# Optimization experiments

Hardware: AMD Instinct MI355X
Metric: run time of the kernel (lower is better)

Reference implementation:

```python
import jax, jax.numpy as jnp
import numpy as np

EPS_DIST = 1e-10
BN_EPS = 1e-5
K = 3  # nsample / three_nn


def setup_inputs() -> dict:
    key = jax.random.key(0)
    ks = jax.random.split(key, 8)
    B, N, S, D1, D2 = 4, 8192, 2048, 128, 256
    C_in = D1 + D2  # 384
    H = 256
    inp = {
        "pos1": jax.random.normal(ks[0], (B, 3, N), dtype=jnp.float32),
        "pos2": jax.random.normal(ks[1], (B, 3, S), dtype=jnp.float32),
        "feature1": jax.random.normal(ks[2], (B, D1, N), dtype=jnp.float32),
        "feature2": jax.random.normal(ks[3], (B, D2, S), dtype=jnp.float32),
        # MLP layer 1: Conv1d(384->256, k=1) + BN
        "W1": jax.random.normal(ks[4], (H, C_in), dtype=jnp.float32) * (1.0 / np.sqrt(C_in)),
        "b1": jnp.zeros((H,), dtype=jnp.float32),
        "g1": jnp.ones((H,), dtype=jnp.float32),
        "be1": jnp.zeros((H,), dtype=jnp.float32),
        # MLP layer 2: Conv1d(256->256, k=1) + BN
        "W2": jax.random.normal(ks[5], (H, H), dtype=jnp.float32) * (1.0 / np.sqrt(H)),
        "b2": jnp.zeros((H,), dtype=jnp.float32),
        "g2": jnp.ones((H,), dtype=jnp.float32),
        "be2": jnp.zeros((H,), dtype=jnp.float32),
    }
    return inp


def _conv_bn_relu(x, W, b, gamma, beta):
    # x: [B, Cin, N]; 1x1 Conv1d == channel GEMM
    y = jnp.einsum("oc,bcn->bon", W, x) + b[None, :, None]
    # BatchNorm1d in training mode: batch statistics over (B, N)
    mean = jnp.mean(y, axis=(0, 2), keepdims=True)
    var = jnp.mean(jnp.square(y - mean), axis=(0, 2), keepdims=True)
    y = (y - mean) * jax.lax.rsqrt(var + BN_EPS)
    y = y * gamma[None, :, None] + beta[None, :, None]
    return jax.nn.relu(y)


def reference(pos1, pos2, feature1, feature2, W1, b1, g1, be1, W2, b2, g2, be2):
    # pos1: [B,3,N], pos2: [B,3,S], feature1: [B,D1,N], feature2: [B,D2,S]
    p1 = jnp.swapaxes(pos1, 1, 2)  # [B,N,3]
    p2 = jnp.swapaxes(pos2, 1, 2)  # [B,S,3]
    # three_nn: squared-distance 3-NN of each point in p1 among p2
    d2 = (jnp.sum(p1 * p1, -1)[:, :, None]
          + jnp.sum(p2 * p2, -1)[:, None, :]
          - 2.0 * jnp.einsum("bnc,bsc->bns", p1, p2))  # [B,N,S]
    neg_vals, idx = jax.lax.top_k(-d2, K)  # idx: [B,N,3]
    dists = jnp.maximum(-neg_vals, EPS_DIST)  # dists[dists<1e-10]=1e-10
    w = 1.0 / dists
    w = w / jnp.sum(w, -1, keepdims=True)  # [B,N,3]
    # grouping_operation: gather feature2 [B,D,S] by idx -> [B,D,N,3]
    grouped = jax.vmap(lambda f, i: f[:, i])(feature2, idx)
    interpolated = jnp.sum(grouped * w[:, None, :, :], axis=-1)  # [B,D2,N]
    feat = jnp.concatenate([interpolated, feature1], axis=1)  # [B,384,N]
    feat = _conv_bn_relu(feat, W1, b1, g1, be1)
    feat = _conv_bn_relu(feat, W2, b2, g2, be2)
    return feat  # [B,256,N]
```

## Files before the change

### kernel.cpp

```cpp
#include <hip/hip_runtime.h>
#include <hip/hip_bf16.h>
#include <cstdint>

typedef unsigned short u16;
typedef unsigned int u32;
typedef unsigned long long u64;
typedef __bf16 bf16x8 __attribute__((ext_vector_type(8)));
typedef float f32x4 __attribute__((ext_vector_type(4)));
typedef u16 u16x8 __attribute__((ext_vector_type(8)));

#define FPSCALE 1048576.0f
#define FPINV   (1.0f / 1048576.0f)
#define NSLICE 16

__device__ __forceinline__ u16 f2b(float f) {
    unsigned int u = __float_as_uint(f);
    u += 0x7fffu + ((u >> 16) & 1u);
    return (u16)(u >> 16);
}
__device__ __forceinline__ float b2f(u16 h) {
    return __uint_as_float(((unsigned int)h) << 16);
}
__device__ __forceinline__ void async_cp16(void* lds, const void* g) {
    __builtin_amdgcn_global_load_lds((const __attribute__((address_space(1))) void*)g,
                                     (__attribute__((address_space(3))) void*)lds, 16, 0, 0);
}
__device__ __forceinline__ u64 ld_agent_u64(const u64* p) {
    return __hip_atomic_load(p, __ATOMIC_RELAXED, __HIP_MEMORY_SCOPE_AGENT);
}
__device__ __forceinline__ u32 fmono(float f) {
    u32 u = __float_as_uint(f);
    return u ^ (((u32)((int)u >> 31)) | 0x80000000u);
}
__device__ __forceinline__ u64 shfl_xor_u64(u64 v, int mask) {
    u32 lo = (u32)v, hi = (u32)(v >> 32);
    lo = (u32)__shfl_xor((int)lo, mask);
    hi = (u32)__shfl_xor((int)hi, mask);
    return ((u64)hi << 32) | lo;
}
__device__ __forceinline__ void ins3(u64 k, u64& k0, u64& k1, u64& k2) {
    bool c0 = k > k0, c1 = k > k1, c2 = k > k2;
    k2 = c1 ? k1 : (c2 ? k : k2);
    k1 = c0 ? k0 : (c1 ? k : k1);
    k0 = c0 ? k : k0;
}
__device__ __forceinline__ int pkix(int i) { return i + (i >> 6); }

#define NB_NN  2048
#define NB_CVT 160
#define NB_T2  512
#define NB_T1  1024

__global__ __launch_bounds__(256, 4) void prep_kernel(const float* __restrict__ w1,
                                                      const float* __restrict__ w2,
                                                      u16* __restrict__ wb,
                                                      const float* __restrict__ feature2,
                                                      u16* __restrict__ f2t,
                                                      const float* __restrict__ feature1,
                                                      u16* __restrict__ f1t,
                                                      const float* __restrict__ pos1,
                                                      const float* __restrict__ pos2,
                                                      int* __restrict__ idx_out,
                                                      float* __restrict__ w_out,
                                                      u64* __restrict__ SZ) {
    __shared__ __align__(16) char smem[34784];
    int bi = blockIdx.x;
    int tid = threadIdx.x;

    if (bi >= NB_NN) {
        int ci = bi - NB_NN;
        if (ci >= NB_CVT + NB_T2 + NB_T1) {
            for (int i = tid; i < 2 * NSLICE * 512; i += 256) SZ[i] = 0;
            if (tid == 0) *(int*)(SZ + 2 * NSLICE * 512) = 0;
            return;
        }
        if (ci < NB_CVT) {
            int i = ci * 256 + tid;
            if (i < 40960) {
                const float* src = (i < 24576) ? w1 : w2;
                int k = (i < 24576) ? i : (i - 24576);
                float4 v = *(const float4*)&src[(size_t)k * 4];
                ushort4 o;
                o.x = f2b(v.x); o.y = f2b(v.y); o.z = f2b(v.z); o.w = f2b(v.w);
                *(ushort4*)&wb[(size_t)i * 4] = o;
            }
            return;
        }
        float (*t)[65] = (float (*)[65])smem;
        const float* in; u16* out; int C, S, s0, c0, b;
        if (ci < NB_CVT + NB_T2) {
            int lin = ci - NB_CVT;
            C = 256; S = 2048; in = feature2; out = f2t;
            s0 = (lin & 31) * 64; c0 = ((lin >> 5) & 3) * 64; b = lin >> 7;
        } else {
            int lin = ci - NB_CVT - NB_T2;
            C = 128; S = 8192; in = feature1; out = f1t;
            s0 = (lin & 127) * 64; c0 = ((lin >> 7) & 1) * 64; b = lin >> 8;
        }
        const float* ib = in + (size_t)b * C * S;
        u16* ob = out + (size_t)b * S * C;
        int col = tid & 63, r0 = tid >> 6;
#pragma unroll
        for (int p = 0; p < 16; ++p) {
            int c = p * 4 + r0;
            t[c][col] = ib[(size_t)(c0 + c) * S + s0 + col];
        }
        __syncthreads();
#pragma unroll
        for (int p = 0; p < 16; ++p) {
            int s = p * 4 + r0;
            ob[(size_t)(s0 + s) * C + c0 + col] = f2b(t[col][s]);
        }
        return;
    }

    float4* pk = (float4*)smem;
    u64* warr = (u64*)(smem + 33248);
    int j0 = bi * 16;
    int b = j0 >> 13;
    const float* p2 = pos2 + (size_t)b * 3 * 2048;
    int p = tid & 15, ck = tid >> 4;
    int wv = tid >> 6, lane = tid & 63;
    const float* p1 = pos1 + (size_t)b * 3 * 8192;
    int n = (j0 & 8191) + p;
    float qx = p1[n], qy = p1[8192 + n], qz = p1[16384 + n];
    u64 key0 = 0, key1 = 0, key2 = 0;

    for (int i = tid; i < 2048; i += 256) {
        float x = p2[i], y = p2[2048 + i], z = p2[4096 + i];
        pk[pkix(i)] = make_float4(x, y, z, -0.5f * (x * x + y * y + z * z));
    }
    __syncthreads();

    int sb = ck * 128;
#pragma unroll
    for (int h = 0; h < 2; ++h) {
        int cb = sb + h * 64;
        const float4* pc = pk + pkix(cb);
        float ga0 = -3.4e38f, ga1 = -3.4e38f, ga2 = -3.4e38f;
        float gb0 = -3.4e38f, gb1 = -3.4e38f, gb2 = -3.4e38f;
        int ia0 = 0, ia1 = 0, ia2 = 0, ib0 = 0, ib1 = 0, ib2 = 0;
#pragma unroll 4
        for (int it = 0; it < 64; it += 2) {
            float4 cdA = pc[it];
            float4 cdB = pc[it + 1];
            {
                int s = cb + it;
                float tv = fmaf(qx, cdA.x, fmaf(qy, cdA.y, fmaf(qz, cdA.z, cdA.w)));
                bool c0 = tv > ga0, c1 = tv > ga1, c2 = tv > ga2;
                float o0 = ga0, o1 = ga1;
                ga2 = __builtin_amdgcn_fmed3f(tv, o1, ga2);
                ga1 = __builtin_amdgcn_fmed3f(tv, o0, o1);
                ga0 = fmaxf(o0, tv);
                ia2 = c1 ? ia1 : (c2 ? s : ia2);
                ia1 = c0 ? ia0 : (c1 ? s : ia1);
                ia0 = c0 ? s : ia0;
            }
            {
                int s = cb + it + 1;
                float tv = fmaf(qx, cdB.x, fmaf(qy, cdB.y, fmaf(qz, cdB.z, cdB.w)));
                bool c0 = tv > gb0, c1 = tv > gb1, c2 = tv > gb2;
                float o0 = gb0, o1 = gb1;
                gb2 = __builtin_amdgcn_fmed3f(tv, o1, gb2);
                gb1 = __builtin_amdgcn_fmed3f(tv, o0, o1);
                gb0 = fmaxf(o0, tv);
                ib2 = c1 ? ib1 : (c2 ? s : ib2);
                ib1 = c0 ? ib0 : (c1 ? s : ib1);
                ib0 = c0 ? s : ib0;
            }
        }
        ins3(((u64)fmono(ga0) << 32) | (u64)(2047 - ia0), key0, key1, key2);
        ins3(((u64)fmono(ga1) << 32) | (u64)(2047 - ia1), key0, key1, key2);
        ins3(((u64)fmono(ga2) << 32) | (u64)(2047 - ia2), key0, key1, key2);
        ins3(((u64)fmono(gb0) << 32) | (u64)(2047 - ib0), key0, key1, key2);
        ins3(((u64)fmono(gb1) << 32) | (u64)(2047 - ib1), key0, key1, key2);
        ins3(((u64)fmono(gb2) << 32) | (u64)(2047 - ib2), key0, key1, key2);
    }

#pragma unroll
    for (int mask = 16; mask <= 32; mask <<= 1) {
        u64 m0 = shfl_xor_u64(key0, mask);
        u64 m1 = shfl_xor_u64(key1, mask);
        u64 m2 = shfl_xor_u64(key2, mask);
        ins3(m0, key0, key1, key2);
        ins3(m1, key0, key1, key2);
        ins3(m2, key0, key1, key2);
    }
    if (lane < 16) {
        u64* wr = &warr[(wv * 16 + p) * 3];
        wr[0] = key0; wr[1] = key1; wr[2] = key2;
    }
    __syncthreads();
    if (tid < 16) {
        int pp = tid;
        const u64* w0 = &warr[pp * 3];
        u64 k0 = w0[0], k1 = w0[1], k2 = w0[2];
#pragma unroll
        for (int w = 1; w < 4; ++w) {
            const u64* wr = &warr[(w * 16 + pp) * 3];
            ins3(wr[0], k0, k1, k2);
            ins3(wr[1], k0, k1, k2);
            ins3(wr[2], k0, k1, k2);
        }
        int s0 = 2047 - (int)(k0 & 0xFFFFFFFFu);
        int s1 = 2047 - (int)(k1 & 0xFFFFFFFFu);
        int s2 = 2047 - (int)(k2 & 0xFFFFFFFFu);
        int j = j0 + pp;
        int nn = j & 8191;
        float x1 = p1[nn], y1 = p1[8192 + nn], z1 = p1[16384 + nn];
        float n1 = x1 * x1 + y1 * y1 + z1 * z1;
        float X0 = p2[s0], Y0 = p2[2048 + s0], Z0 = p2[4096 + s0];
        float X1 = p2[s1], Y1v = p2[2048 + s1], Z1 = p2[4096 + s1];
        float X2 = p2[s2], Y2v = p2[2048 + s2], Z2 = p2[4096 + s2];
        float t0 = x1 * X0 + y1 * Y0 + z1 * Z0 - 0.5f * (X0 * X0 + Y0 * Y0 + Z0 * Z0);
        float t1 = x1 * X1 + y1 * Y1v + z1 * Z1 - 0.5f * (X1 * X1 + Y1v * Y1v + Z1 * Z1);
        float t2 = x1 * X2 + y1 * Y2v + z1 * Z2 - 0.5f * (X2 * X2 + Y2v * Y2v + Z2 * Z2);
        float d0 = fmaxf(fmaf(-2.f, t0, n1), 1e-10f);
        float d1 = fmaxf(fmaf(-2.f, t1, n1), 1e-10f);
        float d2 = fmaxf(fmaf(-2.f, t2, n1), 1e-10f);
        float w0v = 1.f / d0, w1v = 1.f / d1, w2v = 1.f / d2;
        float inv = 1.f / (w0v + w1v + w2v);
        idx_out[j * 3] = s0; idx_out[j * 3 + 1] = s1; idx_out[j * 3 + 2] = s2;
        w_out[j * 3] = w0v * inv; w_out[j * 3 + 1] = w1v * inv; w_out[j * 3 + 2] = w2v * inv;
    }
}

__device__ __forceinline__ void gridbar(int* cnt, int target) {
    __syncthreads();
    if (threadIdx.x == 0) {
        __hip_atomic_fetch_add(cnt, 1, __ATOMIC_RELAXED, __HIP_MEMORY_SCOPE_AGENT);
        while (__hip_atomic_load(cnt, __ATOMIC_RELAXED, __HIP_MEMORY_SCOPE_AGENT) < target)
            __builtin_amdgcn_s_sleep(16);
        __atomic_signal_fence(__ATOMIC_SEQ_CST);
    }
    __syncthreads();
}

__global__ __launch_bounds__(512, 1) void mlp_fused(const u16* __restrict__ F2T,
                                                    const int* __restrict__ idx,
                                                    const float* __restrict__ wgt,
                                                    const u16* __restrict__ A2g,
                                                    const u16* __restrict__ W1b,
                                                    const float* __restrict__ b1,
                                                    const u16* __restrict__ W2b,
                                                    const float* __restrict__ b2,
                                                    u64* __restrict__ S1,
                                                    const float* __restrict__ g1,
                                                    const float* __restrict__ be1,
                                                    u64* __restrict__ S2,
                                                    const float* __restrict__ g2,
                                                    const float* __restrict__ be2,
                                                    float* __restrict__ OUT,
                                                    int* __restrict__ BAR) {
    __shared__ __align__(16) char smem[141312];
    u16* AS  = (u16*)smem;
    u16* BS  = (u16*)(smem + 32768);
    u16* A2  = (u16*)smem;
    u16* BS2 = (u16*)(smem + 65536);
    float* SC  = (float*)(smem + 131072);
    float* SC2 = (float*)(smem + 135168);
    float2* BNT = (float2*)(smem + 139264);

    int tid = threadIdx.x, bid = blockIdx.x;
    int lane = tid & 63, wv = tid >> 6;
    int l15 = lane & 15, q = lane >> 4;
    int lrow = lane >> 3, lchunk = lane & 7, schunk = lchunk ^ lrow;
    int j0 = bid * 128;
    int rw = wv & 3;
    int cg = wv >> 2;
    int wrow = rw * 32;
    int cbase = cg * 128;
    int sl = (bid & (NSLICE - 1)) * 512;

    const u16* gp0[2]; const u16* gp1[2]; const u16* gp2[2];
    float gw0[2], gw1[2], gw2[2];
#pragma unroll
    for (int qq = 0; qq < 2; ++qq) {
        int r = wv * 16 + qq * 8 + lrow;
        int j = j0 + r;
        int bb = j >> 13;
        const u16* fb = F2T + (size_t)bb * 2048 * 256;
        gp0[qq] = fb + (size_t)idx[j * 3 + 0] * 256;
        gp1[qq] = fb + (size_t)idx[j * 3 + 1] * 256;
        gp2[qq] = fb + (size_t)idx[j * 3 + 2] * 256;
        gw0[qq] = wgt[j * 3 + 0]; gw1[qq] = wgt[j * 3 + 1]; gw2[qq] = wgt[j * 3 + 2];
    }
    u16x8 G0[2], G1[2], G2[2];

    f32x4 acc[2][8];
#pragma unroll
    for (int i = 0; i < 2; ++i)
#pragma unroll
        for (int jj = 0; jj < 8; ++jj) acc[i][jj] = (f32x4){0.f, 0.f, 0.f, 0.f};

    auto stageB1 = [&](int buf, int k0) {
#pragma unroll
        for (int qq = 0; qq < 4; ++qq) {
            int row = wv * 32 + qq * 8;
            async_cp16(&BS[buf * 16384 + row * 64],
                       W1b + (size_t)(row + lrow) * 384 + k0 + schunk * 8);
        }
    };
    auto stageA1f1 = [&](int buf, int k0) {
        const u16* src = A2g + (size_t)j0 * 128 + (k0 - 256);
#pragma unroll
        for (int qq = 0; qq < 2; ++qq) {
            int row = wv * 16 + qq * 8;
            async_cp16(&AS[buf * 8192 + row * 64],
                       src + (size_t)(row + lrow) * 128 + schunk * 8);
        }
    };
    auto gissue = [&](int k0) {
        int c = k0 + lchunk * 8;
#pragma unroll
        for (int qq = 0; qq < 2; ++qq) {
            G0[qq] = *(const u16x8*)(gp0[qq] + c);
            G1[qq] = *(const u16x8*)(gp1[qq] + c);
            G2[qq] = *(const u16x8*)(gp2[qq] + c);
        }
    };
    auto gwrite = [&](int buf) {
#pragma unroll
        for (int qq = 0; qq < 2; ++qq) {
            int row = wv * 16 + qq * 8;
            u16x8 o;
#pragma unroll
            for (int e = 0; e < 8; ++e)
                o[e] = f2b(gw0[qq] * b2f(G0[qq][e]) + gw1[qq] * b2f(G1[qq][e]) +
                           gw2[qq] * b2f(G2[qq][e]));
            *(u16x8*)&AS[buf * 8192 + (row + lrow) * 64 + schunk * 8] = o;
        }
    };
    auto stageB2 = [&](int buf, int k0) {
#pragma unroll
        for (int qq = 0; qq < 4; ++qq) {
            int row = wv * 32 + qq * 8;
            async_cp16(&BS2[buf * 16384 + row * 64],
                       W2b + (size_t)(row + lrow) * 256 + k0 + schunk * 8);
        }
    };

    gissue(0);
    stageB1(0, 0);
    gwrite(0);
    __syncthreads();
    for (int t = 0; t < 6; ++t) {
        int cur = t & 1;
        if (t < 3) { gissue((t + 1) * 64); stageB1(cur ^ 1, (t + 1) * 64); }
        else if (t < 5) { stageB1(cur ^ 1, (t + 1) * 64); stageA1f1(cur ^ 1, (t + 1) * 64); }
#pragma unroll
        for (int ks = 0; ks < 2; ++ks) {
            bf16x8 af[2];
#pragma unroll
            for (int i = 0; i < 2; ++i) {
                int row = wrow + i * 16 + l15;
                af[i] = *(const bf16x8*)&AS[cur * 8192 + row * 64 +
                                            ((ks * 4 + q) ^ (l15 & 7)) * 8];
            }
#pragma unroll
            for (int jj = 0; jj < 8; ++jj) {
                int brow = cbase + jj * 16 + l15;
                bf16x8 bfr = *(const bf16x8*)&BS[cur * 16384 + brow * 64 +
                                                 ((ks * 4 + q) ^ (l15 & 7)) * 8];
#pragma unroll
                for (int i = 0; i < 2; ++i)
                    acc[i][jj] = __builtin_amdgcn_mfma_f32_16x16x32_bf16(af[i], bfr,
                                                                         acc[i][jj], 0, 0, 0);
            }
        }
        if (t < 3) gwrite(cur ^ 1);
        __syncthreads();
    }

    stageB2(0, 0);

#pragma unroll
    for (int jj = 0; jj < 8; ++jj) {
        int c = cbase + jj * 16 + l15;
        float bv = b1[c];
        float s = 0.f, s2 = 0.f;
#pragma unroll
        for (int i = 0; i < 2; ++i)
#pragma unroll
            for (int r = 0; r < 4; ++r) {
                acc[i][jj][r] += bv;
                float v = acc[i][jj][r];
                s += v; s2 += v * v;
            }
        s += __shfl_xor(s, 16); s += __shfl_xor(s, 32);
        s2 += __shfl_xor(s2, 16); s2 += __shfl_xor(s2, 32);
        if (q == 0) { SC[rw * 256 + c] = s; SC2[rw * 256 + c] = s2; }
    }
    __syncthreads();
    if (tid < 256) {
        float fs = SC[tid] + SC[256 + tid] + SC[512 + tid] + SC[768 + tid];
        float fs2 = SC2[tid] + SC2[256 + tid] + SC2[512 + tid] + SC2[768 + tid];
        atomicAdd(&S1[sl + tid], (u64)(long long)llrintf(fs * FPSCALE));
        atomicAdd(&S1[sl + 256 + tid], (u64)(long long)llrintf(fs2 * FPSCALE));
    }
    gridbar(BAR, 256);

    if (tid < 256) {
        long long su = 0, sq = 0;
#pragma unroll
        for (int r = 0; r < NSLICE; ++r) {
            su += (long long)ld_agent_u64(&S1[r * 512 + tid]);
            sq += (long long)ld_agent_u64(&S1[r * 512 + 256 + tid]);
        }
        float fs = (float)su * FPINV;
        float fs2 = (float)sq * FPINV;
        const float inv = 1.f / 32768.f;
        float mean = fs * inv;
        float var = fs2 * inv - mean * mean;
        float a = g1[tid] * rsqrtf(var + 1e-5f);
        BNT[tid] = make_float2(a, be1[tid] - mean * a);
    }
    __syncthreads();

#pragma unroll
    for (int jj = 0; jj < 8; ++jj) {
        int c = cbase + jj * 16 + l15;
        float2 bn = BNT[c];
        int chunkbase = c >> 3;
        int win = c & 7;
#pragma unroll
        for (int i = 0; i < 2; ++i)
#pragma unroll
            for (int r = 0; r < 4; ++r) {
                int row = wrow + i * 16 + q * 4 + r;
                float vb = b2f(f2b(acc[i][jj][r]));
                u16 h = f2b(fmaxf(vb * bn.x + bn.y, 0.f));
                A2[row * 256 + ((chunkbase ^ (row & 7)) * 8 + win)] = h;
            }
    }
    __syncthreads();

#pragma unroll
    for (int i = 0; i < 2; ++i)
#pragma unroll
        for (int jj = 0; jj < 8; ++jj) acc[i][jj] = (f32x4){0.f, 0.f, 0.f, 0.f};

    for (int t = 0; t < 4; ++t) {
        int cur = t & 1;
        if (t < 3) stageB2(cur ^ 1, (t + 1) * 64);
#pragma unroll
        for (int ks = 0; ks < 2; ++ks) {
            bf16x8 af[2];
            int kc = t * 8 + ks * 4 + q;
#pragma unroll
            for (int i = 0; i < 2; ++i) {
                int row = wrow + i * 16 + l15;
                af[i] = *(const bf16x8*)&A2[row * 256 + ((kc ^ (l15 & 7)) * 8)];
            }
#pragma unroll
            for (int jj = 0; jj < 8; ++jj) {
                int brow = cbase + jj * 16 + l15;
                bf16x8 bfr = *(const bf16x8*)&BS2[cur * 16384 + brow * 64 +
                                                  ((ks * 4 + q) ^ (l15 & 7)) * 8];
#pragma unroll
                for (int i = 0; i < 2; ++i)
                    acc[i][jj] = __builtin_amdgcn_mfma_f32_16x16x32_bf16(af[i], bfr,
                                                                         acc[i][jj], 0, 0, 0);
            }
        }
        __syncthreads();
    }

#pragma unroll
    for (int jj = 0; jj < 8; ++jj) {
        int c = cbase + jj * 16 + l15;
        float bv = b2[c];
        float s = 0.f, s2 = 0.f;
#pragma unroll
        for (int i = 0; i < 2; ++i)
#pragma unroll
            for (int r = 0; r < 4; ++r) {
                acc[i][jj][r] += bv;
                float v = acc[i][jj][r];
                s += v; s2 += v * v;
            }
        s += __shfl_xor(s, 16); s += __shfl_xor(s, 32);
        s2 += __shfl_xor(s2, 16); s2 += __shfl_xor(s2, 32);
        if (q == 0) { SC[rw * 256 + c] = s; SC2[rw * 256 + c] = s2; }
    }
    __syncthreads();
    if (tid < 256) {
        float fs = SC[tid] + SC[256 + tid] + SC[512 + tid] + SC[768 + tid];
        float fs2 = SC2[tid] + SC2[256 + tid] + SC2[512 + tid] + SC2[768 + tid];
        atomicAdd(&S2[sl + tid], (u64)(long long)llrintf(fs * FPSCALE));
        atomicAdd(&S2[sl + 256 + tid], (u64)(long long)llrintf(fs2 * FPSCALE));
    }
    gridbar(BAR, 512);

    if (tid < 256) {
        long long su = 0, sq = 0;
#pragma unroll
        for (int r = 0; r < NSLICE; ++r) {
            su += (long long)ld_agent_u64(&S2[r * 512 + tid]);
            sq += (long long)ld_agent_u64(&S2[r * 512 + 256 + tid]);
        }
        float fs = (float)su * FPINV;
        float fs2 = (float)sq * FPINV;
        const float inv = 1.f / 32768.f;
        float mean = fs * inv;
        float var = fs2 * inv - mean * mean;
        float a = g2[tid] * rsqrtf(var + 1e-5f);
        BNT[tid] = make_float2(a, be2[tid] - mean * a);
    }
    __syncthreads();

    int bb = j0 >> 13, nbase = j0 & 8191;
#pragma unroll
    for (int jj = 0; jj < 8; ++jj) {
        int o = cbase + jj * 16 + l15;
        float2 bn = BNT[o];
#pragma unroll
        for (int i = 0; i < 2; ++i) {
            int n0 = nbase + wrow + i * 16 + q * 4;
            float4 v;
            v.x = fmaxf(b2f(f2b(acc[i][jj][0])) * bn.x + bn.y, 0.f);
            v.y = fmaxf(b2f(f2b(acc[i][jj][1])) * bn.x + bn.y, 0.f);
            v.z = fmaxf(b2f(f2b(acc[i][jj][2])) * bn.x + bn.y, 0.f);
            v.w = fmaxf(b2f(f2b(acc[i][jj][3])) * bn.x + bn.y, 0.f);
            *(float4*)&OUT[(size_t)bb * 2097152 + (size_t)o * 8192 + n0] = v;
        }
    }
}

extern "C" void kernel_launch(void* const* d_in, const int* in_sizes, int n_in,
                              void* d_out, int out_size, void* d_ws, size_t ws_size,
                              hipStream_t stream) {
    const float* pos1 = (const float*)d_in[0];
    const float* pos2 = (const float*)d_in[1];
    const float* feature1 = (const float*)d_in[2];
    const float* feature2 = (const float*)d_in[3];
    const float* W1 = (const float*)d_in[4];
    const float* b1 = (const float*)d_in[5];
    const float* g1 = (const float*)d_in[6];
    const float* be1 = (const float*)d_in[7];
    const float* W2 = (const float*)d_in[8];
    const float* b2 = (const float*)d_in[9];
    const float* g2 = (const float*)d_in[10];
    const float* be2 = (const float*)d_in[11];

    char* ws = (char*)d_ws;
    int*    IDX   = (int*)(ws + 0);
    float*  WGT   = (float*)(ws + 393216);
    u16*    W1B   = (u16*)(ws + 786432);
    u16*    W2B   = (u16*)(ws + 983040);
    u16*    F2T   = (u16*)(ws + 1118208);
    u16*    F1T   = (u16*)(ws + 5312512);
    u64*    SSTAT = (u64*)(ws + 47255552);
    u64*    S1    = SSTAT;
    u64*    S2    = SSTAT + NSLICE * 512;
    int*    BAR   = (int*)(SSTAT + 2 * NSLICE * 512);
    float*  OUT   = (float*)d_out;

    prep_kernel<<<NB_NN + NB_CVT + NB_T2 + NB_T1 + 1, 256, 0, stream>>>(
        W1, W2, W1B, feature2, F2T, feature1, F1T, pos1, pos2, IDX, WGT, SSTAT);
    mlp_fused<<<256, 512, 0, stream>>>(F2T, IDX, WGT, F1T, W1B, b1, W2B, b2,
                                       S1, g1, be1, S2, g2, be2, OUT, BAR);
}
```

Before: 169.3 us.

## Fuse three-NN search into MLP kernel and drop global idx/weight round-trip

Moves the brute-force 3-NN search and inverse-distance weight computation from the prep kernel into the fused MLP kernel. Each of the 256 blocks now computes neighbors for its own 128 query points into LDS, so the idx/weight arrays never go through global memory and the prep kernel shrinks to weight conversion and transposes. The cost is that the NN scan now runs on only 256 blocks of 512 threads, each thread scanning 512 candidates instead of 128, so it is less parallel and adds serial latency before the GEMM starts.

```diff
diff --git a/kernel.cpp b/kernel.cpp
--- a/kernel.cpp
+++ b/kernel.cpp
@@ -46,182 +46,62 @@
 }
 __device__ __forceinline__ int pkix(int i) { return i + (i >> 6); }
 
-#define NB_NN  2048
 #define NB_CVT 160
 #define NB_T2  512
 #define NB_T1  1024
 
-__global__ __launch_bounds__(256, 4) void prep_kernel(const float* __restrict__ w1,
+__global__ __launch_bounds__(256, 8) void prep_kernel(const float* __restrict__ w1,
                                                       const float* __restrict__ w2,
                                                       u16* __restrict__ wb,
                                                       const float* __restrict__ feature2,
                                                       u16* __restrict__ f2t,
                                                       const float* __restrict__ feature1,
                                                       u16* __restrict__ f1t,
-                                                      const float* __restrict__ pos1,
-                                                      const float* __restrict__ pos2,
-                                                      int* __restrict__ idx_out,
-                                                      float* __restrict__ w_out,
                                                       u64* __restrict__ SZ) {
-    __shared__ __align__(16) char smem[34784];
-    int bi = blockIdx.x;
+    __shared__ __align__(16) float t[64][65];
+    int ci = blockIdx.x;
     int tid = threadIdx.x;
 
-    if (bi >= NB_NN) {
-        int ci = bi - NB_NN;
-        if (ci >= NB_CVT + NB_T2 + NB_T1) {
-            for (int i = tid; i < 2 * NSLICE * 512; i += 256) SZ[i] = 0;
-            if (tid == 0) *(int*)(SZ + 2 * NSLICE * 512) = 0;
-            return;
-        }
-        if (ci < NB_CVT) {
-            int i = ci * 256 + tid;
-            if (i < 40960) {
-                const float* src = (i < 24576) ? w1 : w2;
-                int k = (i < 24576) ? i : (i - 24576);
-                float4 v = *(const float4*)&src[(size_t)k * 4];
-                ushort4 o;
-                o.x = f2b(v.x); o.y = f2b(v.y); o.z = f2b(v.z); o.w = f2b(v.w);
-                *(ushort4*)&wb[(size_t)i * 4] = o;
-            }
-            return;
-        }
-        float (*t)[65] = (float (*)[65])smem;
-        const float* in; u16* out; int C, S, s0, c0, b;
-        if (ci < NB_CVT + NB_T2) {
-            int lin = ci - NB_CVT;
-            C = 256; S = 2048; in = feature2; out = f2t;
-            s0 = (lin & 31) * 64; c0 = ((lin >> 5) & 3) * 64; b = lin >> 7;
-        } else {
-            int lin = ci - NB_CVT - NB_T2;
-            C = 128; S = 8192; in = feature1; out = f1t;
-            s0 = (lin & 127) * 64; c0 = ((lin >> 7) & 1) * 64; b = lin >> 8;
-        }
-        const float* ib = in + (size_t)b * C * S;
-        u16* ob = out + (size_t)b * S * C;
-        int col = tid & 63, r0 = tid >> 6;
-#pragma unroll
-        for (int p = 0; p < 16; ++p) {
-            int c = p * 4 + r0;
-            t[c][col] = ib[(size_t)(c0 + c) * S + s0 + col];
-        }
-        __syncthreads();
-#pragma unroll
-        for (int p = 0; p < 16; ++p) {
-            int s = p * 4 + r0;
-            ob[(size_t)(s0 + s) * C + c0 + col] = f2b(t[col][s]);
-        }
+    if (ci >= NB_CVT + NB_T2 + NB_T1) {
+        for (int i = tid; i < 2 * NSLICE * 512; i += 256) SZ[i] = 0;
+        if (tid == 0) *(int*)(SZ + 2 * NSLICE * 512) = 0;
         return;
     }
-
-    float4* pk = (float4*)smem;
-    u64* warr = (u64*)(smem + 33248);
-    int j0 = bi * 16;
-    int b = j0 >> 13;
-    const float* p2 = pos2 + (size_t)b * 3 * 2048;
-    int p = tid & 15, ck = tid >> 4;
-    int wv = tid >> 6, lane = tid & 63;
-    const float* p1 = pos1 + (size_t)b * 3 * 8192;
-    int n = (j0 & 8191) + p;
-    float qx = p1[n], qy = p1[8192 + n], qz = p1[16384 + n];
-    u64 key0 = 0, key1 = 0, key2 = 0;
-
-    for (int i = tid; i < 2048; i += 256) {
-        float x = p2[i], y = p2[2048 + i], z = p2[4096 + i];
-        pk[pkix(i)] = make_float4(x, y, z, -0.5f * (x * x + y * y + z * z));
-    }
-    __syncthreads();
-
-    int sb = ck * 128;
-#pragma unroll
-    for (int h = 0; h < 2; ++h) {
-        int cb = sb + h * 64;
-        const float4* pc = pk + pkix(cb);
-        float ga0 = -3.4e38f, ga1 = -3.4e38f, ga2 = -3.4e38f;
-        float gb0 = -3.4e38f, gb1 = -3.4e38f, gb2 = -3.4e38f;
-        int ia0 = 0, ia1 = 0, ia2 = 0, ib0 = 0, ib1 = 0, ib2 = 0;
-#pragma unroll 4
-        for (int it = 0; it < 64; it += 2) {
-            float4 cdA = pc[it];
-            float4 cdB = pc[it + 1];
-            {
-                int s = cb + it;
-                float tv = fmaf(qx, cdA.x, fmaf(qy, cdA.y, fmaf(qz, cdA.z, cdA.w)));
-                bool c0 = tv > ga0, c1 = tv > ga1, c2 = tv > ga2;
-                float o0 = ga0, o1 = ga1;
-                ga2 = __builtin_amdgcn_fmed3f(tv, o1, ga2);
-                ga1 = __builtin_amdgcn_fmed3f(tv, o0, o1);
-                ga0 = fmaxf(o0, tv);
-                ia2 = c1 ? ia1 : (c2 ? s : ia2);
-                ia1 = c0 ? ia0 : (c1 ? s : ia1);
-                ia0 = c0 ? s : ia0;
-            }
-            {
-                int s = cb + it + 1;
-                float tv = fmaf(qx, cdB.x, fmaf(qy, cdB.y, fmaf(qz, cdB.z, cdB.w)));
-                bool c0 = tv > gb0, c1 = tv > gb1, c2 = tv > gb2;
-                float o0 = gb0, o1 = gb1;
-                gb2 = __builtin_amdgcn_fmed3f(tv, o1, gb2);
-                gb1 = __builtin_amdgcn_fmed3f(tv, o0, o1);
-                gb0 = fmaxf(o0, tv);
-                ib2 = c1 ? ib1 : (c2 ? s : ib2);
-                ib1 = c0 ? ib0 : (c1 ? s : ib1);
-                ib0 = c0 ? s : ib0;
-            }
-        }
-        ins3(((u64)fmono(ga0) << 32) | (u64)(2047 - ia0), key0, key1, key2);
-        ins3(((u64)fmono(ga1) << 32) | (u64)(2047 - ia1), key0, key1, key2);
-        ins3(((u64)fmono(ga2) << 32) | (u64)(2047 - ia2), key0, key1, key2);
-        ins3(((u64)fmono(gb0) << 32) | (u64)(2047 - ib0), key0, key1, key2);
-        ins3(((u64)fmono(gb1) << 32) | (u64)(2047 - ib1), key0, key1, key2);
-        ins3(((u64)fmono(gb2) << 32) | (u64)(2047 - ib2), key0, key1, key2);
-    }
-
-#pragma unroll
-    for (int mask = 16; mask <= 32; mask <<= 1) {
-        u64 m0 = shfl_xor_u64(key0, mask);
-        u64 m1 = shfl_xor_u64(key1, mask);
-        u64 m2 = shfl_xor_u64(key2, mask);
-        ins3(m0, key0, key1, key2);
-        ins3(m1, key0, key1, key2);
-        ins3(m2, key0, key1, key2);
-    }
-    if (lane < 16) {
-        u64* wr = &warr[(wv * 16 + p) * 3];
-        wr[0] = key0; wr[1] = key1; wr[2] = key2;
-    }
-    __syncthreads();
-    if (tid < 16) {
-        int pp = tid;
-        const u64* w0 = &warr[pp * 3];
-        u64 k0 = w0[0], k1 = w0[1], k2 = w0[2];
-#pragma unroll
-        for (int w = 1; w < 4; ++w) {
-            const u64* wr = &warr[(w * 16 + pp) * 3];
-            ins3(wr[0], k0, k1, k2);
-            ins3(wr[1], k0, k1, k2);
-            ins3(wr[2], k0, k1, k2);
-        }
-        int s0 = 2047 - (int)(k0 & 0xFFFFFFFFu);
-        int s1 = 2047 - (int)(k1 & 0xFFFFFFFFu);
-        int s2 = 2047 - (int)(k2 & 0xFFFFFFFFu);
-        int j = j0 + pp;
-        int nn = j & 8191;
-        float x1 = p1[nn], y1 = p1[8192 + nn], z1 = p1[16384 + nn];
-        float n1 = x1 * x1 + y1 * y1 + z1 * z1;
-        float X0 = p2[s0], Y0 = p2[2048 + s0], Z0 = p2[4096 + s0];
-        float X1 = p2[s1], Y1v = p2[2048 + s1], Z1 = p2[4096 + s1];
-        float X2 = p2[s2], Y2v = p2[2048 + s2], Z2 = p2[4096 + s2];
-        float t0 = x1 * X0 + y1 * Y0 + z1 * Z0 - 0.5f * (X0 * X0 + Y0 * Y0 + Z0 * Z0);
-        float t1 = x1 * X1 + y1 * Y1v + z1 * Z1 - 0.5f * (X1 * X1 + Y1v * Y1v + Z1 * Z1);
-        float t2 = x1 * X2 + y1 * Y2v + z1 * Z2 - 0.5f * (X2 * X2 + Y2v * Y2v + Z2 * Z2);
-        float d0 = fmaxf(fmaf(-2.f, t0, n1), 1e-10f);
-        float d1 = fmaxf(fmaf(-2.f, t1, n1), 1e-10f);
-        float d2 = fmaxf(fmaf(-2.f, t2, n1), 1e-10f);
-        float w0v = 1.f / d0, w1v = 1.f / d1, w2v = 1.f / d2;
-        float inv = 1.f / (w0v + w1v + w2v);
-        idx_out[j * 3] = s0; idx_out[j * 3 + 1] = s1; idx_out[j * 3 + 2] = s2;
-        w_out[j * 3] = w0v * inv; w_out[j * 3 + 1] = w1v * inv; w_out[j * 3 + 2] = w2v * inv;
+    if (ci < NB_CVT) {
+        int i = ci * 256 + tid;
+        if (i < 40960) {
+            const float* src = (i < 24576) ? w1 : w2;
+            int k = (i < 24576) ? i : (i - 24576);
+            float4 v = *(const float4*)&src[(size_t)k * 4];
+            ushort4 o;
+            o.x = f2b(v.x); o.y = f2b(v.y); o.z = f2b(v.z); o.w = f2b(v.w);
+            *(ushort4*)&wb[(size_t)i * 4] = o;
+        }
+        return;
+    }
+    const float* in; u16* out; int C, S, s0, c0, b;
+    if (ci < NB_CVT + NB_T2) {
+        int lin = ci - NB_CVT;
+        C = 256; S = 2048; in = feature2; out = f2t;
+        s0 = (lin & 31) * 64; c0 = ((lin >> 5) & 3) * 64; b = lin >> 7;
+    } else {
+        int lin = ci - NB_CVT - NB_T2;
+        C = 128; S = 8192; in = feature1; out = f1t;
+        s0 = (lin & 127) * 64; c0 = ((lin >> 7) & 1) * 64; b = lin >> 8;
+    }
+    const float* ib = in + (size_t)b * C * S;
+    u16* ob = out + (size_t)b * S * C;
+    int col = tid & 63, r0 = tid >> 6;
+#pragma unroll
+    for (int p = 0; p < 16; ++p) {
+        int c = p * 4 + r0;
+        t[c][col] = ib[(size_t)(c0 + c) * S + s0 + col];
+    }
+    __syncthreads();
+#pragma unroll
+    for (int p = 0; p < 16; ++p) {
+        int s = p * 4 + r0;
+        ob[(size_t)(s0 + s) * C + c0 + col] = f2b(t[col][s]);
     }
 }
 
@@ -236,9 +116,9 @@
     __syncthreads();
 }
 
-__global__ __launch_bounds__(512, 1) void mlp_fused(const u16* __restrict__ F2T,
-                                                    const int* __restrict__ idx,
-                                                    const float* __restrict__ wgt,
+__global__ __launch_bounds__(512, 1) void mlp_fused(const float* __restrict__ pos1,
+                                                    const float* __restrict__ pos2,
+                                                    const u16* __restrict__ F2T,
                                                     const u16* __restrict__ A2g,
                                                     const u16* __restrict__ W1b,
                                                     const float* __restrict__ b1,
@@ -260,6 +140,9 @@
     float* SC  = (float*)(smem + 131072);
     float* SC2 = (float*)(smem + 135168);
     float2* BNT = (float2*)(smem + 139264);
+    float4* pk  = (float4*)smem;
+    int*   IDXL = (int*)(smem + 33280);
+    float* WGTL = (float*)(smem + 34816);
 
     int tid = threadIdx.x, bid = blockIdx.x;
     int lane = tid & 63, wv = tid >> 6;
@@ -271,20 +154,113 @@
     int wrow = rw * 32;
     int cbase = cg * 128;
     int sl = (bid & (NSLICE - 1)) * 512;
+    int bb = j0 >> 13;
+
+    {
+        const float* p2 = pos2 + (size_t)bb * 6144;
+        const float* p1 = pos1 + (size_t)bb * 24576;
+        for (int i = tid; i < 2048; i += 512) {
+            float x = p2[i], y = p2[2048 + i], z = p2[4096 + i];
+            pk[pkix(i)] = make_float4(x, y, z, -0.5f * (x * x + y * y + z * z));
+        }
+        __syncthreads();
+
+        int p = lane & 15, ck = lane >> 4;
+        int nq = (j0 & 8191) + wv * 16 + p;
+        float qx = p1[nq], qy = p1[8192 + nq], qz = p1[16384 + nq];
+        float ga0 = -3.4e38f, ga1 = -3.4e38f, ga2 = -3.4e38f;
+        float gb0 = -3.4e38f, gb1 = -3.4e38f, gb2 = -3.4e38f;
+        int ia0 = 0, ia1 = 0, ia2 = 0, ib0 = 0, ib1 = 0, ib2 = 0;
+        int sb = ck * 512;
+        for (int h = 0; h < 8; ++h) {
+            int cb = sb + h * 64;
+            const float4* pc = pk + pkix(cb);
+#pragma unroll 4
+            for (int it = 0; it < 64; it += 2) {
+                float4 cdA = pc[it];
+                float4 cdB = pc[it + 1];
+                {
+                    int s = cb + it;
+                    float tv = fmaf(qx, cdA.x, fmaf(qy, cdA.y, fmaf(qz, cdA.z, cdA.w)));
+                    bool c0 = tv > ga0, c1 = tv > ga1, c2 = tv > ga2;
+                    float o0 = ga0, o1 = ga1;
+                    ga2 = __builtin_amdgcn_fmed3f(tv, o1, ga2);
+                    ga1 = __builtin_amdgcn_fmed3f(tv, o0, o1);
+                    ga0 = fmaxf(o0, tv);
+                    ia2 = c1 ? ia1 : (c2 ? s : ia2);
+                    ia1 = c0 ? ia0 : (c1 ? s : ia1);
+                    ia0 = c0 ? s : ia0;
+                }
+                {
+                    int s = cb + it + 1;
+                    float tv = fmaf(qx, cdB.x, fmaf(qy, cdB.y, fmaf(qz, cdB.z, cdB.w)));
+                    bool c0 = tv > gb0, c1 = tv > gb1, c2 = tv > gb2;
+                    float o0 = gb0, o1 = gb1;
+                    gb2 = __builtin_amdgcn_fmed3f(tv, o1, gb2);
+                    gb1 = __builtin_amdgcn_fmed3f(tv, o0, o1);
+                    gb0 = fmaxf(o0, tv);
+                    ib2 = c1 ? ib1 : (c2 ? s : ib2);
+                    ib1 = c0 ? ib0 : (c1 ? s : ib1);
+                    ib0 = c0 ? s : ib0;
+                }
+            }
+        }
+        u64 key0 = 0, key1 = 0, key2 = 0;
+        ins3(((u64)fmono(ga0) << 32) | (u64)(2047 - ia0), key0, key1, key2);
+        ins3(((u64)fmono(ga1) << 32) | (u64)(2047 - ia1), key0, key1, key2);
+        ins3(((u64)fmono(ga2) << 32) | (u64)(2047 - ia2), key0, key1, key2);
+        ins3(((u64)fmono(gb0) << 32) | (u64)(2047 - ib0), key0, key1, key2);
+        ins3(((u64)fmono(gb1) << 32) | (u64)(2047 - ib1), key0, key1, key2);
+        ins3(((u64)fmono(gb2) << 32) | (u64)(2047 - ib2), key0, key1, key2);
+#pragma unroll
+        for (int mask = 16; mask <= 32; mask <<= 1) {
+            u64 m0 = shfl_xor_u64(key0, mask);
+            u64 m1 = shfl_xor_u64(key1, mask);
+            u64 m2 = shfl_xor_u64(key2, mask);
+            ins3(m0, key0, key1, key2);
+            ins3(m1, key0, key1, key2);
+            ins3(m2, key0, key1, key2);
+        }
+        if (lane < 16) {
+            int s0 = 2047 - (int)(key0 & 0xFFFFFFFFu);
+            int s1 = 2047 - (int)(key1 & 0xFFFFFFFFu);
+            int s2 = 2047 - (int)(key2 & 0xFFFFFFFFu);
+            int r = wv * 16 + p;
+            int nn = (j0 & 8191) + r;
+            float x1 = p1[nn], y1 = p1[8192 + nn], z1 = p1[16384 + nn];
+            float n1 = x1 * x1 + y1 * y1 + z1 * z1;
+            float X0 = p2[s0], Y0 = p2[2048 + s0], Z0 = p2[4096 + s0];
+            float X1 = p2[s1], Y1v = p2[2048 + s1], Z1 = p2[4096 + s1];
+            float X2 = p2[s2], Y2v = p2[2048 + s2], Z2 = p2[4096 + s2];
+            float t0 = x1 * X0 + y1 * Y0 + z1 * Z0 - 0.5f * (X0 * X0 + Y0 * Y0 + Z0 * Z0);
+            float t1 = x1 * X1 + y1 * Y1v + z1 * Z1 - 0.5f * (X1 * X1 + Y1v * Y1v + Z1 * Z1);
+            float t2 = x1 * X2 + y1 * Y2v + z1 * Z2 - 0.5f * (X2 * X2 + Y2v * Y2v + Z2 * Z2);
+            float d0 = fmaxf(fmaf(-2.f, t0, n1), 1e-10f);
+            float d1 = fmaxf(fmaf(-2.f, t1, n1), 1e-10f);
+            float d2 = fmaxf(fmaf(-2.f, t2, n1), 1e-10f);
+            float w0v = 1.f / d0, w1v = 1.f / d1, w2v = 1.f / d2;
+            float inv = 1.f / (w0v + w1v + w2v);
+            IDXL[r * 3 + 0] = s0; IDXL[r * 3 + 1] = s1; IDXL[r * 3 + 2] = s2;
+            WGTL[r * 3 + 0] = w0v * inv; WGTL[r * 3 + 1] = w1v * inv; WGTL[r * 3 + 2] = w2v * inv;
+        }
+    }
+    __syncthreads();
 
     const u16* gp0[2]; const u16* gp1[2]; const u16* gp2[2];
     float gw0[2], gw1[2], gw2[2];
-#pragma unroll
-    for (int qq = 0; qq < 2; ++qq) {
-        int r = wv * 16 + qq * 8 + lrow;
-        int j = j0 + r;
-        int bb = j >> 13;
+    {
         const u16* fb = F2T + (size_t)bb * 2048 * 256;
-        gp0[qq] = fb + (size_t)idx[j * 3 + 0] * 256;
-        gp1[qq] = fb + (size_t)idx[j * 3 + 1] * 256;
-        gp2[qq] = fb + (size_t)idx[j * 3 + 2] * 256;
-        gw0[qq] = wgt[j * 3 + 0]; gw1[qq] = wgt[j * 3 + 1]; gw2[qq] = wgt[j * 3 + 2];
-    }
+#pragma unroll
+        for (int qq = 0; qq < 2; ++qq) {
+            int r = wv * 16 + qq * 8 + lrow;
+            gp0[qq] = fb + (size_t)IDXL[r * 3 + 0] * 256;
+            gp1[qq] = fb + (size_t)IDXL[r * 3 + 1] * 256;
+            gp2[qq] = fb + (size_t)IDXL[r * 3 + 2] * 256;
+            gw0[qq] = WGTL[r * 3 + 0]; gw1[qq] = WGTL[r * 3 + 1]; gw2[qq] = WGTL[r * 3 + 2];
+        }
+    }
+    __syncthreads();
+
     u16x8 G0[2], G1[2], G2[2];
 
     f32x4 acc[2][8];
@@ -509,7 +485,7 @@
     }
     __syncthreads();
 
-    int bb = j0 >> 13, nbase = j0 & 8191;
+    int nbase = j0 & 8191;
 #pragma unroll
     for (int jj = 0; jj < 8; ++jj) {
         int o = cbase + jj * 16 + l15;
@@ -544,8 +520,6 @@
     const float* be2 = (const float*)d_in[11];
 
     char* ws = (char*)d_ws;
-    int*    IDX   = (int*)(ws + 0);
-    float*  WGT   = (float*)(ws + 393216);
     u16*    W1B   = (u16*)(ws + 786432);
     u16*    W2B   = (u16*)(ws + 983040);
     u16*    F2T   = (u16*)(ws + 1118208);
@@ -556,8 +530,8 @@
     int*    BAR   = (int*)(SSTAT + 2 * NSLICE * 512);
     float*  OUT   = (float*)d_out;
 
-    prep_kernel<<<NB_NN + NB_CVT + NB_T2 + NB_T1 + 1, 256, 0, stream>>>(
-        W1, W2, W1B, feature2, F2T, feature1, F1T, pos1, pos2, IDX, WGT, SSTAT);
-    mlp_fused<<<256, 512, 0, stream>>>(F2T, IDX, WGT, F1T, W1B, b1, W2B, b2,
+    prep_kernel<<<NB_CVT + NB_T2 + NB_T1 + 1, 256, 0, stream>>>(
+        W1, W2, W1B, feature2, F2T, feature1, F1T, SSTAT);
+    mlp_fused<<<256, 512, 0, stream>>>(pos1, pos2, F2T, F1T, W1B, b1, W2B, b2,
                                        S1, g1, be1, S2, g2, be2, OUT, BAR);
 }
```

Result: no change. 168.9 us (median of 2 runs) (-0.2%).
